# Optimization experiments

Measured on AMD Instinct MI355X. Metric: run time of the kernel, lower is better.

The kernel has to match this reference:

```python
import jax, jax.numpy as jnp
import numpy as np

E = 8        # num_experts
TOPK = 2     # num_experts_per_tok
H = 2048     # hidden_size
I = 1024     # intermediate_size (c_fc outputs 2*I because is_glu)
STD = 0.02


def setup_inputs() -> dict:
    key = jax.random.key(0)
    k1, k2, k3, k4 = jax.random.split(key, 4)
    return {
        "x": jax.random.normal(k1, (4, 2048, H), jnp.float32),
        "w_gate": jax.random.normal(k2, (E, H), jnp.float32) * STD,
        "w_fc": jax.random.normal(k3, (E, 2 * I, H), jnp.float32) * STD,
        "w_proj": jax.random.normal(k4, (E, H, I), jnp.float32) * STD,
    }


def reference(x, w_gate, w_fc, w_proj):
    orig_shape = x.shape
    xf = x.reshape(-1, H)                      # [T, H]
    T = xf.shape[0]

    # routing
    router_logits = xf @ w_gate.T              # [T, E]
    top_vals, top_idx = jax.lax.top_k(router_logits, TOPK)   # [T, K]
    router_weights = jax.nn.softmax(top_vals.astype(jnp.float32), axis=-1).astype(x.dtype)

    # combine weights: [T, E], zero for unselected experts (top-k indices are distinct)
    combine = jnp.zeros((T, E), x.dtype).at[jnp.arange(T)[:, None], top_idx].set(router_weights)

    # per-expert FFN; equivalent to sort/scatter grouped GEMM since unselected
    # tokens get zero combine weight. scan over the small fixed expert axis
    # keeps peak memory to one [T, 2I] intermediate.
    def body(y, ewc):
        wfc_e, wproj_e, c_e = ewc              # [2I,H], [H,I], [T]
        h = xf @ wfc_e.T                       # [T, 2I]
        a, b = jnp.split(h, 2, axis=-1)
        h = jax.nn.silu(a) * b                 # GLU: [T, I]
        y = y + c_e[:, None] * (h @ wproj_e.T)
        return y, None

    y0 = jnp.zeros_like(xf)
    y, _ = jax.lax.scan(body, y0, (w_fc, w_proj, combine.T))
    return y.reshape(orig_shape), router_logits
```

## Files before the change

### kernel.cpp

```cpp
#include <hip/hip_runtime.h>
#include <hip/hip_bf16.h>
#include <stdint.h>

#define T_TOK 8192
#define HID   2048
#define IM    1024
#define NE    8
#define NASSIGN (T_TOK*2)

typedef __attribute__((ext_vector_type(8))) short bf16x8;
typedef __attribute__((ext_vector_type(4))) float f32x4;

__device__ __forceinline__ void gload16(void* lds, const void* g) {
  __builtin_amdgcn_global_load_lds((const __attribute__((address_space(1))) char*)g,
                                   (__attribute__((address_space(3))) char*)lds, 16, 0, 0);
}

__device__ __forceinline__ ushort f2b(float f) {
  union { float f; uint32_t u; } c; c.f = f;
  uint32_t u = c.u;
  return (ushort)((u + 0x7FFFu + ((u >> 16) & 1u)) >> 16);
}

__global__ void cast_kernel(const float* __restrict__ in, ushort* __restrict__ out, int n4) {
  int i = blockIdx.x * blockDim.x + threadIdx.x;
  int stride = gridDim.x * blockDim.x;
  for (; i < n4; i += stride) {
    float4 v = ((const float4*)in)[i];
    ushort4 o;
    o.x = f2b(v.x); o.y = f2b(v.y); o.z = f2b(v.z); o.w = f2b(v.w);
    ((ushort4*)out)[i] = o;
  }
}

__global__ __launch_bounds__(256) void router_kernel(
    const float* __restrict__ x, const float* __restrict__ wg,
    float* __restrict__ logits_out, int4* __restrict__ recI, float2* __restrict__ recW,
    int* __restrict__ counts) {
  int wid = threadIdx.x >> 6, lane = threadIdx.x & 63;
  int tok = blockIdx.x * 4 + wid;
  if (tok >= T_TOK) return;
  const float4* xr = (const float4*)(x + (size_t)tok * HID);
  float4 xv[8];
#pragma unroll
  for (int j = 0; j < 8; ++j) xv[j] = xr[j * 64 + lane];
  float lf[NE];
#pragma unroll
  for (int e = 0; e < NE; ++e) {
    const float4* wrow = (const float4*)(wg + (size_t)e * HID);
    double acc = 0.0;
#pragma unroll
    for (int j = 0; j < 8; ++j) {
      float4 w4 = wrow[j * 64 + lane];
      acc += (double)xv[j].x * w4.x + (double)xv[j].y * w4.y +
             (double)xv[j].z * w4.z + (double)xv[j].w * w4.w;
    }
#pragma unroll
    for (int off = 32; off; off >>= 1) acc += __shfl_xor(acc, off);
    lf[e] = (float)acc;
  }
  if (lane == 0) {
#pragma unroll
    for (int e = 0; e < NE; ++e) logits_out[(size_t)tok * NE + e] = lf[e];
    int i1 = 0;
#pragma unroll
    for (int e = 1; e < NE; ++e) if (lf[e] > lf[i1]) i1 = e;
    int i2 = -1;
#pragma unroll
    for (int e = 0; e < NE; ++e) {
      if (e == i1) continue;
      if (i2 < 0 || lf[e] > lf[i2]) i2 = e;
    }
    float t = expf(lf[i2] - lf[i1]);
    float w1 = 1.0f / (1.0f + t);
    float w2 = t / (1.0f + t);
    int s1 = atomicAdd(&counts[i1], 1);
    int s2 = atomicAdd(&counts[i2], 1);
    recI[tok] = make_int4(i1, s1, i2, s2);
    recW[tok] = make_float2(w1, w2);
  }
}

__global__ void scan_kernel(const int* __restrict__ counts, int* __restrict__ offs) {
  int s = 0;
  for (int e = 0; e < NE; ++e) { offs[e] = s; s += counts[e]; }
  offs[NE] = s;
}

__global__ void scatter_kernel(const int4* __restrict__ recI, const float2* __restrict__ recW,
                               const int* __restrict__ offs,
                               int* __restrict__ tok_id, float* __restrict__ aw) {
  int t = blockIdx.x * blockDim.x + threadIdx.x;
  if (t >= T_TOK) return;
  int4 r = recI[t]; float2 w = recW[t];
  int p1 = offs[r.x] + r.y; tok_id[p1] = t; aw[p1] = w.x;
  int p2 = offs[r.z] + r.w; tok_id[p2] = t; aw[p2] = w.y;
}

__global__ __launch_bounds__(256, 2) void gemm1_kernel(
    const ushort* __restrict__ xb, const ushort* __restrict__ wfcb,
    const int* __restrict__ tok_id, const float* __restrict__ aw,
    const int* __restrict__ counts, const int* __restrict__ offs,
    ushort* __restrict__ hglu) {
  int bid = blockIdx.x;
  int e = bid >> 10;
  int rem = bid & 1023;
  int rt = rem >> 4;
  int ct = rem & 15;
  int cnt = counts[e];
  if (rt * 128 >= cnt) return;
  int off = offs[e];
  int tid = threadIdx.x;

  __shared__ ushort As[2][128 * 32];
  __shared__ ushort Ba[2][64 * 32];
  __shared__ ushort Bb[2][64 * 32];

  int tokA[2];
#pragma unroll
  for (int p = 0; p < 2; ++p) {
    int row = (p * 256 + tid) >> 2;
    int slot = rt * 128 + row;
    tokA[p] = tok_id[off + (slot < cnt ? slot : cnt - 1)];
  }
  const size_t wbase_a = ((size_t)e * 2048 + (size_t)ct * 64) * HID;
  const size_t wbase_b = wbase_a + (size_t)1024 * HID;

  auto stage = [&](int b, int kt) {
    int k0 = kt * 32;
#pragma unroll
    for (int p = 0; p < 2; ++p) {
      int s = p * 256 + tid;
      gload16(&As[b][s * 8], xb + (size_t)tokA[p] * HID + k0 + (s & 3) * 8);
    }
    {
      int s = tid;
      size_t rk = (size_t)(s >> 2) * HID + k0 + (s & 3) * 8;
      gload16(&Ba[b][s * 8], wfcb + wbase_a + rk);
      gload16(&Bb[b][s * 8], wfcb + wbase_b + rk);
    }
  };

  int wid = tid >> 6, lane = tid & 63;
  int wr = wid >> 1, wc = wid & 1;
  int q = lane >> 4, r = lane & 15;

  f32x4 accA[4][2] = {};
  f32x4 accB[4][2] = {};

  stage(0, 0);
  __syncthreads();
  for (int kt = 0; kt < HID / 32; ++kt) {
    int cur = kt & 1;
    if (kt < HID / 32 - 1) stage(cur ^ 1, kt + 1);
    bf16x8 af[4], baf[2], bbf[2];
#pragma unroll
    for (int m = 0; m < 4; ++m)
      af[m] = *(const bf16x8*)&As[cur][(wr * 64 + m * 16 + r) * 32 + q * 8];
#pragma unroll
    for (int n = 0; n < 2; ++n) {
      baf[n] = *(const bf16x8*)&Ba[cur][(wc * 32 + n * 16 + r) * 32 + q * 8];
      bbf[n] = *(const bf16x8*)&Bb[cur][(wc * 32 + n * 16 + r) * 32 + q * 8];
    }
#pragma unroll
    for (int m = 0; m < 4; ++m)
#pragma unroll
      for (int n = 0; n < 2; ++n) {
        accA[m][n] = __builtin_amdgcn_mfma_f32_16x16x32_bf16(af[m], baf[n], accA[m][n], 0, 0, 0);
        accB[m][n] = __builtin_amdgcn_mfma_f32_16x16x32_bf16(af[m], bbf[n], accB[m][n], 0, 0, 0);
      }
    __syncthreads();
  }

#pragma unroll
  for (int m = 0; m < 4; ++m) {
    int rowbase = rt * 128 + wr * 64 + m * 16 + q * 4;
#pragma unroll
    for (int j = 0; j < 4; ++j) {
      int slot = rowbase + j;
      if (slot >= cnt) continue;
      float w = aw[off + slot];
      size_t rp = (size_t)(off + slot) * IM + ct * 64 + wc * 32 + r;
#pragma unroll
      for (int n = 0; n < 2; ++n) {
        float a = accA[m][n][j], b = accB[m][n][j];
        float g = (a / (1.0f + expf(-a))) * b * w;
        hglu[rp + n * 16] = f2b(g);
      }
    }
  }
}

__global__ __launch_bounds__(256, 2) void gemm2_kernel(
    const ushort* __restrict__ hglu, const ushort* __restrict__ wpb,
    const int* __restrict__ tok_id,
    const int* __restrict__ counts, const int* __restrict__ offs,
    float* __restrict__ y) {
  int bid = blockIdx.x;
  int e = bid >> 10;
  int rem = bid & 1023;
  int rt = rem >> 4;
  int ct = rem & 15;
  int cnt = counts[e];
  if (rt * 128 >= cnt) return;
  int off = offs[e];
  int tid = threadIdx.x;

  __shared__ ushort As[2][128 * 32];
  __shared__ ushort Bs[2][128 * 32];

  const size_t abase = (size_t)(off + rt * 128) * IM;
  const size_t bbase = ((size_t)e * 2048 + (size_t)ct * 128) * IM;

  auto stage = [&](int b, int kt) {
    int k0 = kt * 32;
#pragma unroll
    for (int p = 0; p < 2; ++p) {
      int s = p * 256 + tid;
      size_t rk = (size_t)(s >> 2) * IM + k0 + (s & 3) * 8;
      gload16(&As[b][s * 8], hglu + abase + rk);
      gload16(&Bs[b][s * 8], wpb + bbase + rk);
    }
  };

  int wid = tid >> 6, lane = tid & 63;
  int wr = wid >> 1, wc = wid & 1;
  int q = lane >> 4, r = lane & 15;

  f32x4 acc[4][4] = {};

  stage(0, 0);
  __syncthreads();
  for (int kt = 0; kt < IM / 32; ++kt) {
    int cur = kt & 1;
    if (kt < IM / 32 - 1) stage(cur ^ 1, kt + 1);
    bf16x8 af[4], bf[4];
#pragma unroll
    for (int m = 0; m < 4; ++m)
      af[m] = *(const bf16x8*)&As[cur][(wr * 64 + m * 16 + r) * 32 + q * 8];
#pragma unroll
    for (int n = 0; n < 4; ++n)
      bf[n] = *(const bf16x8*)&Bs[cur][(wc * 64 + n * 16 + r) * 32 + q * 8];
#pragma unroll
    for (int m = 0; m < 4; ++m)
#pragma unroll
      for (int n = 0; n < 4; ++n)
        acc[m][n] = __builtin_amdgcn_mfma_f32_16x16x32_bf16(af[m], bf[n], acc[m][n], 0, 0, 0);
    __syncthreads();
  }

#pragma unroll
  for (int m = 0; m < 4; ++m) {
    int rowbase = rt * 128 + wr * 64 + m * 16 + q * 4;
#pragma unroll
    for (int j = 0; j < 4; ++j) {
      int slot = rowbase + j;
      if (slot >= cnt) continue;
      int tok = tok_id[off + slot];
      size_t yp = (size_t)tok * HID + ct * 128 + wc * 64 + r;
#pragma unroll
      for (int n = 0; n < 4; ++n)
        atomicAdd(&y[yp + n * 16], acc[m][n][j]);
    }
  }
}

extern "C" void kernel_launch(void* const* d_in, const int* in_sizes, int n_in,
                              void* d_out, int out_size, void* d_ws, size_t ws_size,
                              hipStream_t stream) {
  const float* x     = (const float*)d_in[0];
  const float* wg    = (const float*)d_in[1];
  const float* wfc   = (const float*)d_in[2];
  const float* wproj = (const float*)d_in[3];
  float* y = (float*)d_out;
  float* logits = y + (size_t)T_TOK * HID;

  char* ws = (char*)d_ws;
  ushort* xb   = (ushort*)(ws + 0);
  ushort* wfcb = (ushort*)(ws + 33554432);
  ushort* wpb  = (ushort*)(ws + 100663296);
  ushort* hglu = (ushort*)(ws + 134217728);
  int*    tok  = (int*)   (ws + 168034304);
  float*  aw   = (float*) (ws + 168099840);
  int4*   recI = (int4*)  (ws + 168165376);
  float2* recW = (float2*)(ws + 168296448);
  int*  counts = (int*)   (ws + 168361984);
  int*  offs   = (int*)   (ws + 168362048);
  if (ws_size < 168362112) return;

  hipMemsetAsync(y, 0, (size_t)T_TOK * HID * sizeof(float), stream);
  hipMemsetAsync(counts, 0, NE * sizeof(int), stream);

  cast_kernel<<<2048, 256, 0, stream>>>(x,     xb,   T_TOK * HID / 4);
  cast_kernel<<<4096, 256, 0, stream>>>(wfc,   wfcb, NE * 2 * IM * HID / 4);
  cast_kernel<<<2048, 256, 0, stream>>>(wproj, wpb,  NE * HID * IM / 4);

  router_kernel<<<T_TOK / 4, 256, 0, stream>>>(x, wg, logits, recI, recW, counts);
  scan_kernel<<<1, 1, 0, stream>>>(counts, offs);
  scatter_kernel<<<(T_TOK + 255) / 256, 256, 0, stream>>>(recI, recW, offs, tok, aw);

  gemm1_kernel<<<NE * 64 * 16, 256, 0, stream>>>(xb, wfcb, tok, aw, counts, offs, hglu);
  gemm2_kernel<<<NE * 64 * 16, 256, 0, stream>>>(hglu, wpb, tok, counts, offs, y);
}
```

Before: 898.8 us.

## Split routing into first/second-choice buckets to drop output atomics and memset

Assignments are bucketed by expert and by rank (top-1 or top-2). Each token then appears exactly once per rank, so gemm2 runs twice: the first pass stores directly into y and the second pass adds with a plain read-modify-write. This removes the 64 MB zero-fill of y and the fp32 atomicAdds in the epilogue. The cost is an extra kernel launch, two serialized passes with smaller per-expert tiles that leave more partial tiles, and a second read of y.

```diff
diff --git a/kernel.cpp b/kernel.cpp
--- a/kernel.cpp
+++ b/kernel.cpp
@@ -6,7 +6,6 @@
 #define HID   2048
 #define IM    1024
 #define NE    8
-#define NASSIGN (T_TOK*2)
 
 typedef __attribute__((ext_vector_type(8))) short bf16x8;
 typedef __attribute__((ext_vector_type(4))) float f32x4;
@@ -36,7 +35,7 @@
 __global__ __launch_bounds__(256) void router_kernel(
     const float* __restrict__ x, const float* __restrict__ wg,
     float* __restrict__ logits_out, int4* __restrict__ recI, float2* __restrict__ recW,
-    int* __restrict__ counts) {
+    int* __restrict__ counts2) {
   int wid = threadIdx.x >> 6, lane = threadIdx.x & 63;
   int tok = blockIdx.x * 4 + wid;
   if (tok >= T_TOK) return;
@@ -74,42 +73,47 @@
     float t = expf(lf[i2] - lf[i1]);
     float w1 = 1.0f / (1.0f + t);
     float w2 = t / (1.0f + t);
-    int s1 = atomicAdd(&counts[i1], 1);
-    int s2 = atomicAdd(&counts[i2], 1);
+    int s1 = atomicAdd(&counts2[i1 * 2 + 0], 1);
+    int s2 = atomicAdd(&counts2[i2 * 2 + 1], 1);
     recI[tok] = make_int4(i1, s1, i2, s2);
     recW[tok] = make_float2(w1, w2);
   }
 }
 
-__global__ void scan_kernel(const int* __restrict__ counts, int* __restrict__ offs) {
+__global__ void scan_kernel(const int* __restrict__ counts2, int* __restrict__ offs2,
+                            int* __restrict__ ecnt, int* __restrict__ eoff) {
   int s = 0;
-  for (int e = 0; e < NE; ++e) { offs[e] = s; s += counts[e]; }
-  offs[NE] = s;
+  for (int b = 0; b < 2 * NE; ++b) { offs2[b] = s; s += counts2[b]; }
+  offs2[2 * NE] = s;
+  for (int e = 0; e < NE; ++e) {
+    eoff[e] = offs2[2 * e];
+    ecnt[e] = counts2[2 * e] + counts2[2 * e + 1];
+  }
 }
 
 __global__ void scatter_kernel(const int4* __restrict__ recI, const float2* __restrict__ recW,
-                               const int* __restrict__ offs,
+                               const int* __restrict__ offs2,
                                int* __restrict__ tok_id, float* __restrict__ aw) {
   int t = blockIdx.x * blockDim.x + threadIdx.x;
   if (t >= T_TOK) return;
   int4 r = recI[t]; float2 w = recW[t];
-  int p1 = offs[r.x] + r.y; tok_id[p1] = t; aw[p1] = w.x;
-  int p2 = offs[r.z] + r.w; tok_id[p2] = t; aw[p2] = w.y;
+  int p1 = offs2[r.x * 2 + 0] + r.y; tok_id[p1] = t; aw[p1] = w.x;
+  int p2 = offs2[r.z * 2 + 1] + r.w; tok_id[p2] = t; aw[p2] = w.y;
 }
 
 __global__ __launch_bounds__(256, 2) void gemm1_kernel(
     const ushort* __restrict__ xb, const ushort* __restrict__ wfcb,
     const int* __restrict__ tok_id, const float* __restrict__ aw,
-    const int* __restrict__ counts, const int* __restrict__ offs,
+    const int* __restrict__ ecnt, const int* __restrict__ eoff,
     ushort* __restrict__ hglu) {
   int bid = blockIdx.x;
   int e = bid >> 10;
   int rem = bid & 1023;
   int rt = rem >> 4;
   int ct = rem & 15;
-  int cnt = counts[e];
-  if (rt * 128 >= cnt) return;
-  int off = offs[e];
+  int cnt = ecnt[e];
+  if (cnt == 0 || rt * 128 >= cnt) return;
+  int off = eoff[e];
   int tid = threadIdx.x;
 
   __shared__ ushort As[2][128 * 32];
@@ -194,16 +198,16 @@
 __global__ __launch_bounds__(256, 2) void gemm2_kernel(
     const ushort* __restrict__ hglu, const ushort* __restrict__ wpb,
     const int* __restrict__ tok_id,
-    const int* __restrict__ counts, const int* __restrict__ offs,
-    float* __restrict__ y) {
+    const int* __restrict__ counts2, const int* __restrict__ offs2,
+    float* __restrict__ y, int pass) {
   int bid = blockIdx.x;
   int e = bid >> 10;
   int rem = bid & 1023;
   int rt = rem >> 4;
   int ct = rem & 15;
-  int cnt = counts[e];
-  if (rt * 128 >= cnt) return;
-  int off = offs[e];
+  int cnt = counts2[2 * e + pass];
+  if (cnt == 0 || rt * 128 >= cnt) return;
+  int off = offs2[2 * e + pass];
   int tid = threadIdx.x;
 
   __shared__ ushort As[2][128 * 32];
@@ -257,10 +261,14 @@
       int slot = rowbase + j;
       if (slot >= cnt) continue;
       int tok = tok_id[off + slot];
-      size_t yp = (size_t)tok * HID + ct * 128 + wc * 64 + r;
-#pragma unroll
-      for (int n = 0; n < 4; ++n)
-        atomicAdd(&y[yp + n * 16], acc[m][n][j]);
+      float* yp = &y[(size_t)tok * HID + ct * 128 + wc * 64 + r];
+      if (pass == 0) {
+#pragma unroll
+        for (int n = 0; n < 4; ++n) yp[n * 16] = acc[m][n][j];
+      } else {
+#pragma unroll
+        for (int n = 0; n < 4; ++n) yp[n * 16] += acc[m][n][j];
+      }
     }
   }
 }
@@ -276,29 +284,31 @@
   float* logits = y + (size_t)T_TOK * HID;
 
   char* ws = (char*)d_ws;
-  ushort* xb   = (ushort*)(ws + 0);
-  ushort* wfcb = (ushort*)(ws + 33554432);
-  ushort* wpb  = (ushort*)(ws + 100663296);
-  ushort* hglu = (ushort*)(ws + 134217728);
-  int*    tok  = (int*)   (ws + 168034304);
-  float*  aw   = (float*) (ws + 168099840);
-  int4*   recI = (int4*)  (ws + 168165376);
-  float2* recW = (float2*)(ws + 168296448);
-  int*  counts = (int*)   (ws + 168361984);
-  int*  offs   = (int*)   (ws + 168362048);
-  if (ws_size < 168362112) return;
-
-  hipMemsetAsync(y, 0, (size_t)T_TOK * HID * sizeof(float), stream);
-  hipMemsetAsync(counts, 0, NE * sizeof(int), stream);
+  ushort* xb    = (ushort*)(ws + 0);
+  ushort* wfcb  = (ushort*)(ws + 33554432);
+  ushort* wpb   = (ushort*)(ws + 100663296);
+  ushort* hglu  = (ushort*)(ws + 134217728);
+  int*    tok   = (int*)   (ws + 168034304);
+  float*  aw    = (float*) (ws + 168099840);
+  int4*   recI  = (int4*)  (ws + 168165376);
+  float2* recW  = (float2*)(ws + 168296448);
+  int* counts2  = (int*)   (ws + 168361984);
+  int* offs2    = (int*)   (ws + 168362048);
+  int* ecnt     = (int*)   (ws + 168362120);
+  int* eoff     = (int*)   (ws + 168362152);
+  if (ws_size < 168362184) return;
+
+  hipMemsetAsync(counts2, 0, 2 * NE * sizeof(int), stream);
 
   cast_kernel<<<2048, 256, 0, stream>>>(x,     xb,   T_TOK * HID / 4);
   cast_kernel<<<4096, 256, 0, stream>>>(wfc,   wfcb, NE * 2 * IM * HID / 4);
   cast_kernel<<<2048, 256, 0, stream>>>(wproj, wpb,  NE * HID * IM / 4);
 
-  router_kernel<<<T_TOK / 4, 256, 0, stream>>>(x, wg, logits, recI, recW, counts);
-  scan_kernel<<<1, 1, 0, stream>>>(counts, offs);
-  scatter_kernel<<<(T_TOK + 255) / 256, 256, 0, stream>>>(recI, recW, offs, tok, aw);
-
-  gemm1_kernel<<<NE * 64 * 16, 256, 0, stream>>>(xb, wfcb, tok, aw, counts, offs, hglu);
-  gemm2_kernel<<<NE * 64 * 16, 256, 0, stream>>>(hglu, wpb, tok, counts, offs, y);
-}
+  router_kernel<<<T_TOK / 4, 256, 0, stream>>>(x, wg, logits, recI, recW, counts2);
+  scan_kernel<<<1, 1, 0, stream>>>(counts2, offs2, ecnt, eoff);
+  scatter_kernel<<<(T_TOK + 255) / 256, 256, 0, stream>>>(recI, recW, offs2, tok, aw);
+
+  gemm1_kernel<<<NE * 64 * 16, 256, 0, stream>>>(xb, wfcb, tok, aw, ecnt, eoff, hglu);
+  gemm2_kernel<<<NE * 64 * 16, 256, 0, stream>>>(hglu, wpb, tok, counts2, offs2, y, 0);
+  gemm2_kernel<<<NE * 64 * 16, 256, 0, stream>>>(hglu, wpb, tok, counts2, offs2, y, 1);
+}
```

Measured after the change: 857.1 us. -4.6%, faster.
